# Kernel optimization log

Measured on AMD Instinct MI355X. Metric: run time of the kernel, lower is better.

## Reference

```python
import jax, jax.numpy as jnp
import numpy as np

N = 6144      # total residues (12 complexes x 512)
SEG = 512
NC = 14       # atom channels per residue
E = 64        # embed_size
HD = 128      # hidden_size
C = 25        # num_classes
K = 9         # k_neighbors
L = 3         # n_layers
ROUNDS = 3    # iter_round


def _forward(X, S, batch_id, embed, W_in, b_in, channel_w, eW1, eb1, eW2, eb2, cW1, cb1, cW2, cb2, nW1, nb1, nW2, nb2, mW1, mb1, mW2, mb2, oW1, ob1, oW2, ob2):
    n = X.shape[0]
    silu = jax.nn.silu
    # pairs in different complexes (or self) are never neighbors
    cross = (batch_id[:, None] != batch_id[None, :]) | jnp.eye(n, dtype=bool)
    Hmem = None
    H = None
    for t in range(ROUNDS):
        H0 = embed[S]                                    # residue embedding [N,E]
        if Hmem is not None:                             # keep_memory: memory_ffn(H_prev)
            m = silu(Hmem) @ mW1 + mb1
            H0 = H0 + (silu(m) @ mW2 + mb2)
        H = H0 @ W_in + b_in                             # [N,HD]
        # dynamic KNN edge construction on current CA coordinates (_knn_edges)
        ca = X[:, 1]                                     # [N,3]
        d2 = jnp.sum((ca[:, None, :] - ca[None, :, :]) ** 2, -1)
        d2 = jnp.where(cross, 1e9, d2)
        _, nbr = jax.lax.top_k(-d2, K)                   # [N,K] neighbor indices
        for l in range(L):                               # AMEGNN / AMEncoder layers
            Hj = H[nbr]                                  # gather [N,K,HD]
            Xj = X[nbr]                                  # gather [N,K,NC,3]
            diff = X[:, None] - Xj                       # [N,K,NC,3]
            # channel-weighted radial feature
            radial = jnp.einsum('nkcd,nkcd,c->nk', diff, diff, channel_w)[..., None]
            Hi = jnp.broadcast_to(H[:, None], Hj.shape)
            ein = jnp.concatenate([Hi, Hj, radial], -1)  # [N,K,2HD+1]
            msg = silu(silu(ein @ eW1[l] + eb1[l]) @ eW2[l] + eb2[l])
            scale = silu(msg @ cW1[l] + cb1[l]) @ cW2[l] + cb2[l]     # [N,K,1]
            X = X + jnp.mean(diff * scale[..., None], axis=1)        # equivariant coord update
            agg = jnp.sum(msg, axis=1)                   # scatter-sum over neighbors [N,HD]
            H = H + silu(jnp.concatenate([H, agg], -1) @ nW1[l] + nb1[l]) @ nW2[l] + nb2[l]
        Hmem = H
    logits = silu(silu(H) @ oW1 + ob1) @ oW2 + ob2       # ffn_residue
    return logits, X


def setup_inputs() -> dict:
    key = jax.random.key(0)
    ks = jax.random.split(key, 16)
    r = lambda i, shape, s=0.05: jax.random.normal(ks[i], shape, dtype=jnp.float32) * s
    return {
        'X': jax.random.normal(ks[0], (N, NC, 3), dtype=jnp.float32) * 3.0,
        'S': jax.random.randint(ks[1], (N,), 0, C),
        'batch_id': jnp.arange(N, dtype=jnp.int32) // SEG,
        'embed': r(2, (C, E), 1.0),
        'W_in': r(3, (E, HD)), 'b_in': jnp.zeros((HD,), jnp.float32),
        'channel_w': jax.random.uniform(ks[4], (NC,), dtype=jnp.float32),
        'eW1': r(5, (L, 2 * HD + 1, HD)), 'eb1': jnp.zeros((L, HD), jnp.float32),
        'eW2': r(6, (L, HD, HD)), 'eb2': jnp.zeros((L, HD), jnp.float32),
        'cW1': r(7, (L, HD, HD)), 'cb1': jnp.zeros((L, HD), jnp.float32),
        'cW2': r(8, (L, HD, 1)), 'cb2': jnp.zeros((L, 1), jnp.float32),
        'nW1': r(9, (L, 2 * HD, HD)), 'nb1': jnp.zeros((L, HD), jnp.float32),
        'nW2': r(10, (L, HD, HD)), 'nb2': jnp.zeros((L, HD), jnp.float32),
        'mW1': r(11, (HD, HD)), 'mb1': jnp.zeros((HD,), jnp.float32),
        'mW2': r(12, (HD, E)), 'mb2': jnp.zeros((E,), jnp.float32),
        'oW1': r(13, (HD, HD)), 'ob1': jnp.zeros((HD,), jnp.float32),
        'oW2': r(14, (HD, C)), 'ob2': jnp.zeros((C,), jnp.float32),
    }


def reference(X, S, batch_id, embed, W_in, b_in, channel_w, eW1, eb1, eW2, eb2, cW1, cb1, cW2, cb2, nW1, nb1, nW2, nb2, mW1, mb1, mW2, mb2, oW1, ob1, oW2, ob2):
    return _forward(X, S, batch_id, embed, W_in, b_in, channel_w, eW1, eb1, eW2, eb2, cW1, cb1, cW2, cb2, nW1, nb1, nW2, nb2, mW1, mb1, mW2, mb2, oW1, ob1, oW2, ob2)
```

## Files before the change

kernel.cpp:

```cpp
#include <hip/hip_runtime.h>
#include <math.h>

#define NNODE 6144
#define SEG   512
#define NCH   14
#define XD    42
#define ED    64
#define HD    128
#define NCLS  25
#define KN    9
#define NPB   7
#define ROWS  64
#define EDGE_BLOCKS ((NNODE + NPB - 1) / NPB)

typedef __attribute__((ext_vector_type(8))) short short8;
typedef __attribute__((ext_vector_type(4))) short short4v;
typedef __attribute__((ext_vector_type(4))) float f32x4;

__device__ __forceinline__ float silu_f(float x) {
  return x / (1.0f + __expf(-x));
}
__device__ __forceinline__ short f2bf(float x) {
  unsigned u = __builtin_bit_cast(unsigned, x);
  unsigned r = (u + 0x7fffu + ((u >> 16) & 1u)) >> 16;
  return (short)r;
}
__device__ __forceinline__ float bf2f(short s) {
  unsigned u = ((unsigned)(unsigned short)s) << 16;
  return __builtin_bit_cast(float, u);
}
__device__ __forceinline__ f32x4 mfma16(short8 a, short8 b, f32x4 c) {
  return __builtin_amdgcn_mfma_f32_16x16x32_bf16(a, b, c, 0, 0, 0);
}
__device__ __forceinline__ int swz128(int row, int col) {
  return row * 128 + (col ^ ((row & 7) << 3));
}
__device__ __forceinline__ int swz256(int row, int col) {
  return row * 256 + (col ^ ((row & 7) << 3));
}

__global__ __launch_bounds__(256) void prep_weights(
    const float* __restrict__ eW1, const float* __restrict__ eW2,
    const float* __restrict__ cW1, const float* __restrict__ nW1,
    const float* __restrict__ nW2, short* __restrict__ out)
{
  const int mat = blockIdx.y % 5, l = blockIdx.y / 5;
  const int idx = blockIdx.x * 256 + threadIdx.x;
  const int K = (mat == 0 || mat == 3) ? 256 : 128;
  if (idx >= K * 128) return;
  const int n = idx / K, k = idx - n * K;
  const float* src;
  switch (mat) {
    case 0: src = eW1 + (size_t)l * 257 * 128; break;
    case 1: src = eW2 + (size_t)l * 128 * 128; break;
    case 2: src = cW1 + (size_t)l * 128 * 128; break;
    case 3: src = nW1 + (size_t)l * 256 * 128; break;
    default: src = nW2 + (size_t)l * 128 * 128; break;
  }
  const int dofs[5] = {0, 32768, 49152, 65536, 98304};
  out[(size_t)l * 114688 + dofs[mat] + idx] = f2bf(src[k * 128 + n]);
}

__global__ void copy_kernel(const float* __restrict__ src, float* __restrict__ dst, int n) {
  int i = blockIdx.x * blockDim.x + threadIdx.x;
  if (i < n) dst[i] = src[i];
}

__global__ __launch_bounds__(512) void pq_kernel(
    const float* __restrict__ Hin, const short* __restrict__ W1T,
    float* __restrict__ PQ)
{
  __shared__ __align__(16) short A[32 * HD];
  const int t = threadIdx.x;
  const int m0 = blockIdx.x * 32;

  const float4* H4 = (const float4*)(Hin + (size_t)m0 * HD);
  for (int idx = t; idx < 32 * 32; idx += 512) {
    const int r = idx >> 5, c4 = idx & 31;
    float4 v = H4[r * 32 + c4];
    short4v s;
    s.x = f2bf(v.x); s.y = f2bf(v.y); s.z = f2bf(v.z); s.w = f2bf(v.w);
    *(short4v*)&A[swz128(r, c4 * 4)] = s;
  }
  __syncthreads();

  const int wid = t >> 6, lane = t & 63;
  const int lr = lane & 15, lk = lane >> 4;
  const int mt = wid >> 2;
  const int nb = (wid & 3) * 4;
  const int rA = mt * 16 + lr;

  f32x4 acc[4] = {};
#pragma unroll
  for (int ks = 0; ks < 4; ++ks) {
    const int k0 = ks * 32 + lk * 8;
    const short8 a = *(const short8*)&A[swz128(rA, k0)];
#pragma unroll
    for (int ni = 0; ni < 4; ++ni) {
      const int c = (nb + ni) * 16 + lr;
      const short* bp = (c < HD) ? (W1T + c * 256 + k0)
                                 : (W1T + (c - HD) * 256 + HD + k0);
      const short8 b = *(const short8*)bp;
      acc[ni] = mfma16(a, b, acc[ni]);
    }
  }
#pragma unroll
  for (int ni = 0; ni < 4; ++ni) {
    const int c = (nb + ni) * 16 + lr;
#pragma unroll
    for (int g = 0; g < 4; ++g) {
      const int row = mt * 16 + lk * 4 + g;
      PQ[(size_t)(m0 + row) * 256 + c] = acc[ni][g];
    }
  }
}

__global__ __launch_bounds__(128) void h_init_kernel(
    const float* __restrict__ embed, const int* __restrict__ S,
    const float* __restrict__ W_in, const float* __restrict__ b_in,
    const float* __restrict__ Hmem,
    const float* __restrict__ mW1, const float* __restrict__ mb1,
    const float* __restrict__ mW2, const float* __restrict__ mb2,
    float* __restrict__ Hout)
{
  __shared__ float a1[HD];
  __shared__ float a2[HD];
  __shared__ float h0[ED];
  const int i = blockIdx.x, j = threadIdx.x;

  if (Hmem) {
    a1[j] = silu_f(Hmem[i * HD + j]);
    __syncthreads();
    float m0 = 0.f, m1 = 0.f, m2 = 0.f, m3 = 0.f;
    for (int k = 0; k < HD; k += 4) {
      m0 = fmaf(a1[k + 0], mW1[(k + 0) * HD + j], m0);
      m1 = fmaf(a1[k + 1], mW1[(k + 1) * HD + j], m1);
      m2 = fmaf(a1[k + 2], mW1[(k + 2) * HD + j], m2);
      m3 = fmaf(a1[k + 3], mW1[(k + 3) * HD + j], m3);
    }
    a2[j] = silu_f(mb1[j] + ((m0 + m1) + (m2 + m3)));
    __syncthreads();
    if (j < ED) {
      float v0 = 0.f, v1 = 0.f, v2 = 0.f, v3 = 0.f;
      for (int k = 0; k < HD; k += 4) {
        v0 = fmaf(a2[k + 0], mW2[(k + 0) * ED + j], v0);
        v1 = fmaf(a2[k + 1], mW2[(k + 1) * ED + j], v1);
        v2 = fmaf(a2[k + 2], mW2[(k + 2) * ED + j], v2);
        v3 = fmaf(a2[k + 3], mW2[(k + 3) * ED + j], v3);
      }
      h0[j] = embed[S[i] * ED + j] + mb2[j] + ((v0 + v1) + (v2 + v3));
    }
  } else {
    if (j < ED) h0[j] = embed[S[i] * ED + j];
  }
  __syncthreads();
  float h0a = 0.f, h1a = 0.f, h2a = 0.f, h3a = 0.f;
  for (int k = 0; k < ED; k += 4) {
    h0a = fmaf(h0[k + 0], W_in[(k + 0) * HD + j], h0a);
    h1a = fmaf(h0[k + 1], W_in[(k + 1) * HD + j], h1a);
    h2a = fmaf(h0[k + 2], W_in[(k + 2) * HD + j], h2a);
    h3a = fmaf(h0[k + 3], W_in[(k + 3) * HD + j], h3a);
  }
  Hout[i * HD + j] = b_in[j] + ((h0a + h1a) + (h2a + h3a));
}

__global__ __launch_bounds__(256) void knn_kernel(const float* __restrict__ X,
                                                  int* __restrict__ nbr)
{
  const int w = threadIdx.x >> 6, lane = threadIdx.x & 63;
  const int i = blockIdx.x * 4 + w;
  const int base = (i / SEG) * SEG;

  const float cx = X[i * XD + 3], cy = X[i * XD + 4], cz = X[i * XD + 5];
  float dv[8];
  int   di[8];
#pragma unroll
  for (int q = 0; q < 8; ++q) {
    const int j = base + lane + q * 64;
    float dx = __fsub_rn(cx, X[j * XD + 3]);
    float dy = __fsub_rn(cy, X[j * XD + 4]);
    float dz = __fsub_rn(cz, X[j * XD + 5]);
    float d2 = __fadd_rn(__fadd_rn(__fmul_rn(dx, dx), __fmul_rn(dy, dy)), __fmul_rn(dz, dz));
    if (j == i) d2 = 1e9f;
    dv[q] = d2; di[q] = j;
  }
  for (int it = 0; it < KN; ++it) {
    float bv = dv[0]; int bi = di[0];
#pragma unroll
    for (int q = 1; q < 8; ++q)
      if (dv[q] < bv || (dv[q] == bv && di[q] < bi)) { bv = dv[q]; bi = di[q]; }
#pragma unroll
    for (int m = 1; m < 64; m <<= 1) {
      float ov = __shfl_xor(bv, m, 64);
      int   oi = __shfl_xor(bi, m, 64);
      if (ov < bv || (ov == bv && oi < bi)) { bv = ov; bi = oi; }
    }
    if (lane == 0) nbr[i * KN + it] = bi;
    const int rel = bi - base;
    const int oq = rel >> 6;
#pragma unroll
    for (int q = 0; q < 8; ++q)
      if (q == oq && (rel & 63) == lane) dv[q] = 3e38f;
  }
}

__global__ __launch_bounds__(512, 8) void edge_layer_kernel(
    const float* __restrict__ Hin,  float* __restrict__ Hout,
    const float* __restrict__ Xin,  float* __restrict__ Xout,
    const int*   __restrict__ nbr,  const float* __restrict__ channel_w,
    const float* __restrict__ PQ,
    const float* __restrict__ eW1,  const float* __restrict__ eb1,
    const float* __restrict__ eb2,  const float* __restrict__ cb1,
    const float* __restrict__ cW2,  const float* __restrict__ cb2,
    const float* __restrict__ nb1,  const float* __restrict__ nb2,
    const short* __restrict__ W2T,  const short* __restrict__ C1T,
    const short* __restrict__ N1T,  const short* __restrict__ N2T)
{
  __shared__ __align__(16) short bufA[ROWS * HD];
  __shared__ __align__(16) short bufB[ROWS * HD];
  __shared__ __align__(16) short nodeA[NPB * 256];
  __shared__ __align__(16) short uT[NPB * HD];
  __shared__ float XiS[NPB][XD];
  __shared__ float scaleS[ROWS];
  __shared__ int   nbrS[ROWS];

  const int t  = threadIdx.x;
  const int n0 = blockIdx.x * NPB;
  const int nvalid = (NNODE - n0 < NPB) ? (NNODE - n0) : NPB;
  const int evalid = nvalid * KN;

  {
    const int row  = t >> 3;
    const int part = t & 7;
    const bool rvalid = row < evalid;
    const int nd = row / KN;
    const int jn = rvalid ? nbr[n0 * KN + row] : n0;
    if (part == 0) nbrS[row] = jn;

    float r = 0.f;
    if (rvalid) {
      const float* xi = Xin + (size_t)(n0 + nd) * XD;
      const float* xj = Xin + (size_t)jn * XD;
      {
        const int c = part;
        float dx = xi[c * 3 + 0] - xj[c * 3 + 0];
        float dy = xi[c * 3 + 1] - xj[c * 3 + 1];
        float dz = xi[c * 3 + 2] - xj[c * 3 + 2];
        r += channel_w[c] * (dx * dx + dy * dy + dz * dz);
      }
      if (part < 6) {
        const int c = part + 8;
        float dx = xi[c * 3 + 0] - xj[c * 3 + 0];
        float dy = xi[c * 3 + 1] - xj[c * 3 + 1];
        float dz = xi[c * 3 + 2] - xj[c * 3 + 2];
        r += channel_w[c] * (dx * dx + dy * dy + dz * dz);
      }
    }
    r += __shfl_xor(r, 1, 64);
    r += __shfl_xor(r, 2, 64);
    r += __shfl_xor(r, 4, 64);

    {
      float* XiSf = &XiS[0][0];
      for (int idx = t; idx < NPB * XD; idx += 512) {
        const int nd2 = idx / XD;
        XiSf[idx] = (nd2 < nvalid) ? Xin[n0 * XD + idx] : 0.f;
      }
      for (int idx = t; idx < NPB * HD; idx += 512) {
        const int r2 = idx >> 7, c = idx & 127;
        const float v = (r2 < nvalid) ? Hin[(size_t)(n0 + r2) * HD + c] : 0.f;
        nodeA[swz256(r2, c)] = f2bf(v);
      }
    }

    const int inode = n0 + ((nd < nvalid) ? nd : 0);
    const float4* PQ4 = (const float4*)PQ;
    const float4* w2564 = (const float4*)(eW1 + 256 * HD);
    const float4* eb14 = (const float4*)eb1;
#pragma unroll
    for (int ii = 0; ii < 4; ++ii) {
      const int c4 = part + ii * 8;
      const float4 p = PQ4[(size_t)inode * 64 + c4];
      const float4 q = PQ4[(size_t)jn * 64 + 32 + c4];
      const float4 w = w2564[c4];
      const float4 bb = eb14[c4];
      short4v s;
      s.x = f2bf(silu_f(p.x + q.x + r * w.x + bb.x));
      s.y = f2bf(silu_f(p.y + q.y + r * w.y + bb.y));
      s.z = f2bf(silu_f(p.z + q.z + r * w.z + bb.z));
      s.w = f2bf(silu_f(p.w + q.w + r * w.w + bb.w));
      *(short4v*)&bufA[swz128(row, c4 * 4)] = s;
    }
  }
  __syncthreads();

  const int wid  = t >> 6;
  const int lane = t & 63;
  const int m2 = wid >> 2;
  const int n2 = wid & 3;
  const int lr = lane & 15;
  const int lk = lane >> 4;
  const int rA0 = (m2 * 2) * 16 + lr;
  const int rA1 = rA0 + 16;

  {
    f32x4 acc[2][2] = {};
    const short* b0p = W2T + ((n2 * 2) * 16 + lr) * 128;
    const short* b1p = b0p + 16 * 128;
#pragma unroll
    for (int ks = 0; ks < 4; ++ks) {
      const int k0 = ks * 32 + lk * 8;
      const short8 a0 = *(const short8*)&bufA[swz128(rA0, k0)];
      const short8 a1 = *(const short8*)&bufA[swz128(rA1, k0)];
      const short8 b0 = *(const short8*)(b0p + k0);
      const short8 b1 = *(const short8*)(b1p + k0);
      acc[0][0] = mfma16(a0, b0, acc[0][0]);
      acc[0][1] = mfma16(a0, b1, acc[0][1]);
      acc[1][0] = mfma16(a1, b0, acc[1][0]);
      acc[1][1] = mfma16(a1, b1, acc[1][1]);
    }
#pragma unroll
    for (int ni = 0; ni < 2; ++ni) {
      const int col = (n2 * 2 + ni) * 16 + lr;
      const float bias = eb2[col];
#pragma unroll
      for (int mi = 0; mi < 2; ++mi) {
        const int rb = (m2 * 2 + mi) * 16 + lk * 4;
#pragma unroll
        for (int g = 0; g < 4; ++g)
          bufB[swz128(rb + g, col)] = f2bf(silu_f(acc[mi][ni][g] + bias));
      }
    }
  }
  __syncthreads();

  {
    f32x4 acc[2][2] = {};
    const short* b0p = C1T + ((n2 * 2) * 16 + lr) * 128;
    const short* b1p = b0p + 16 * 128;
#pragma unroll
    for (int ks = 0; ks < 4; ++ks) {
      const int k0 = ks * 32 + lk * 8;
      const short8 a0 = *(const short8*)&bufB[swz128(rA0, k0)];
      const short8 a1 = *(const short8*)&bufB[swz128(rA1, k0)];
      const short8 b0 = *(const short8*)(b0p + k0);
      const short8 b1 = *(const short8*)(b1p + k0);
      acc[0][0] = mfma16(a0, b0, acc[0][0]);
      acc[0][1] = mfma16(a0, b1, acc[0][1]);
      acc[1][0] = mfma16(a1, b0, acc[1][0]);
      acc[1][1] = mfma16(a1, b1, acc[1][1]);
    }
#pragma unroll
    for (int ni = 0; ni < 2; ++ni) {
      const int col = (n2 * 2 + ni) * 16 + lr;
      const float bias = cb1[col];
#pragma unroll
      for (int mi = 0; mi < 2; ++mi) {
        const int rb = (m2 * 2 + mi) * 16 + lk * 4;
#pragma unroll
        for (int g = 0; g < 4; ++g)
          bufA[swz128(rb + g, col)] = f2bf(silu_f(acc[mi][ni][g] + bias));
      }
    }
  }
  __syncthreads();

  {
    const int row = t >> 3, part = t & 7;
    float s = 0.f;
#pragma unroll
    for (int qq = 0; qq < 16; ++qq) {
      const int k = part * 16 + qq;
      s = fmaf(bf2f(bufA[swz128(row, k)]), cW2[k], s);
    }
    s += __shfl_xor(s, 1, 64);
    s += __shfl_xor(s, 2, 64);
    s += __shfl_xor(s, 4, 64);
    if (part == 0) scaleS[row] = s + cb2[0];
  }
  for (int idx = t; idx < NPB * HD; idx += 512) {
    const int r2 = idx >> 7, col = idx & 127;
    float v = 0.f;
    if (r2 < nvalid) {
#pragma unroll
      for (int k = 0; k < KN; ++k) v += bf2f(bufB[swz128(r2 * KN + k, col)]);
    }
    nodeA[swz256(r2, col + HD)] = f2bf(v);
  }
  __syncthreads();

  {
    f32x4 acc = {};
    const short* bp = N1T + (wid * 16 + lr) * 256;
#pragma unroll
    for (int ks = 0; ks < 8; ++ks) {
      const int k0 = ks * 32 + lk * 8;
      short8 a = {0, 0, 0, 0, 0, 0, 0, 0};
      if (lr < NPB) a = *(const short8*)&nodeA[swz256(lr, k0)];
      const short8 b = *(const short8*)(bp + k0);
      acc = mfma16(a, b, acc);
    }
    const int col = wid * 16 + lr;
    const float bias = nb1[col];
#pragma unroll
    for (int g = 0; g < 4; ++g) {
      const int orow = lk * 4 + g;
      if (orow < NPB) uT[swz128(orow, col)] = f2bf(silu_f(acc[g] + bias));
    }
  }
  {
    float* XiSf = &XiS[0][0];
    for (int idx = t; idx < NPB * XD; idx += 512) {
      const int nd = idx / XD, e = idx - nd * XD;
      if (nd < nvalid) {
        const float xi = XiSf[idx];
        float a = 0.f;
#pragma unroll
        for (int k = 0; k < KN; ++k) {
          const int r = nd * KN + k;
          a += (xi - Xin[(size_t)nbrS[r] * XD + e]) * scaleS[r];
        }
        Xout[(size_t)(n0 + nd) * XD + e] = xi + a / 9.0f;
      }
    }
  }
  __syncthreads();

  {
    f32x4 acc = {};
    const short* bp = N2T + (wid * 16 + lr) * 128;
#pragma unroll
    for (int ks = 0; ks < 4; ++ks) {
      const int k0 = ks * 32 + lk * 8;
      short8 a = {0, 0, 0, 0, 0, 0, 0, 0};
      if (lr < NPB) a = *(const short8*)&uT[swz128(lr, k0)];
      const short8 b = *(const short8*)(bp + k0);
      acc = mfma16(a, b, acc);
    }
    const int col = wid * 16 + lr;
    const float bias = nb2[col];
#pragma unroll
    for (int g = 0; g < 4; ++g) {
      const int row = lk * 4 + g;
      if (row < nvalid)
        Hout[(size_t)(n0 + row) * HD + col] =
            Hin[(size_t)(n0 + row) * HD + col] + acc[g] + bias;
    }
  }
}

__global__ __launch_bounds__(128) void out_kernel(
    const float* __restrict__ H, const float* __restrict__ X,
    const float* __restrict__ oW1, const float* __restrict__ ob1,
    const float* __restrict__ oW2, const float* __restrict__ ob2,
    float* __restrict__ out)
{
  __shared__ float hs[HD];
  __shared__ float u[HD];
  const int i = blockIdx.x, j = threadIdx.x;

  hs[j] = silu_f(H[i * HD + j]);
  __syncthreads();
  float a0 = 0.f, a1 = 0.f, a2 = 0.f, a3 = 0.f;
  for (int k = 0; k < HD; k += 4) {
    a0 = fmaf(hs[k + 0], oW1[(k + 0) * HD + j], a0);
    a1 = fmaf(hs[k + 1], oW1[(k + 1) * HD + j], a1);
    a2 = fmaf(hs[k + 2], oW1[(k + 2) * HD + j], a2);
    a3 = fmaf(hs[k + 3], oW1[(k + 3) * HD + j], a3);
  }
  u[j] = silu_f(ob1[j] + ((a0 + a1) + (a2 + a3)));
  __syncthreads();
  if (j < NCLS) {
    float o0 = 0.f, o1 = 0.f, o2 = 0.f, o3 = 0.f;
    for (int k = 0; k < HD; k += 4) {
      o0 = fmaf(u[k + 0], oW2[(k + 0) * NCLS + j], o0);
      o1 = fmaf(u[k + 1], oW2[(k + 1) * NCLS + j], o1);
      o2 = fmaf(u[k + 2], oW2[(k + 2) * NCLS + j], o2);
      o3 = fmaf(u[k + 3], oW2[(k + 3) * NCLS + j], o3);
    }
    out[i * NCLS + j] = ob2[j] + ((o0 + o1) + (o2 + o3));
  }
  if (j < XD) out[NNODE * NCLS + i * XD + j] = X[i * XD + j];
}

extern "C" void kernel_launch(void* const* d_in, const int* in_sizes, int n_in,
                              void* d_out, int out_size, void* d_ws, size_t ws_size,
                              hipStream_t stream)
{
  const float* X0       = (const float*)d_in[0];
  const int*   S        = (const int*)  d_in[1];
  const float* embed    = (const float*)d_in[3];
  const float* W_in     = (const float*)d_in[4];
  const float* b_in     = (const float*)d_in[5];
  const float* channelw = (const float*)d_in[6];
  const float* eW1      = (const float*)d_in[7];
  const float* eb1      = (const float*)d_in[8];
  const float* eW2      = (const float*)d_in[9];
  const float* eb2      = (const float*)d_in[10];
  const float* cW1      = (const float*)d_in[11];
  const float* cb1      = (const float*)d_in[12];
  const float* cW2      = (const float*)d_in[13];
  const float* cb2      = (const float*)d_in[14];
  const float* nW1      = (const float*)d_in[15];
  const float* nb1      = (const float*)d_in[16];
  const float* nW2      = (const float*)d_in[17];
  const float* nb2      = (const float*)d_in[18];
  const float* mW1      = (const float*)d_in[19];
  const float* mb1      = (const float*)d_in[20];
  const float* mW2      = (const float*)d_in[21];
  const float* mb2      = (const float*)d_in[22];
  const float* oW1      = (const float*)d_in[23];
  const float* ob1      = (const float*)d_in[24];
  const float* oW2      = (const float*)d_in[25];
  const float* ob2      = (const float*)d_in[26];

  char* ws = (char*)d_ws;
  const size_t HBYTES = (size_t)NNODE * HD * sizeof(float);
  const size_t XBYTES = (size_t)NNODE * XD * sizeof(float);
  float* Hb[2] = { (float*)(ws), (float*)(ws + HBYTES) };
  float* Xb[2] = { (float*)(ws + 2 * HBYTES), (float*)(ws + 2 * HBYTES + XBYTES) };
  int*   nbr   = (int*)(ws + 2 * HBYTES + 2 * XBYTES);
  short* Wbf   = (short*)(ws + 2 * HBYTES + 2 * XBYTES + (size_t)NNODE * KN * sizeof(int));
  float* PQ    = (float*)(ws + 2 * HBYTES + 2 * XBYTES + (size_t)NNODE * KN * sizeof(int)
                             + 3 * 114688 * sizeof(short));

  prep_weights<<<dim3(128, 15), 256, 0, stream>>>(eW1, eW2, cW1, nW1, nW2, Wbf);
  copy_kernel<<<(NNODE * XD + 255) / 256, 256, 0, stream>>>(X0, Xb[0], NNODE * XD);

  int hc = 0, xc = 0;
  for (int t = 0; t < 3; ++t) {
    const float* Hmem = (t == 0) ? nullptr : Hb[hc];
    h_init_kernel<<<NNODE, HD, 0, stream>>>(embed, S, W_in, b_in, Hmem,
                                            mW1, mb1, mW2, mb2, Hb[hc ^ 1]);
    hc ^= 1;
    knn_kernel<<<NNODE / 4, 256, 0, stream>>>(Xb[xc], nbr);
    for (int l = 0; l < 3; ++l) {
      const short* Wl = Wbf + (size_t)l * 114688;
      pq_kernel<<<NNODE / 32, 512, 0, stream>>>(Hb[hc], Wl, PQ);
      edge_layer_kernel<<<EDGE_BLOCKS, 512, 0, stream>>>(
          Hb[hc], Hb[hc ^ 1], Xb[xc], Xb[xc ^ 1], nbr, channelw, PQ,
          eW1 + (size_t)l * 257 * HD, eb1 + (size_t)l * HD,
          eb2 + (size_t)l * HD,  cb1 + (size_t)l * HD,
          cW2 + (size_t)l * HD,  cb2 + (size_t)l,
          nb1 + (size_t)l * HD,  nb2 + (size_t)l * HD,
          Wl + 32768, Wl + 49152, Wl + 65536, Wl + 98304);
      hc ^= 1; xc ^= 1;
    }
  }
  out_kernel<<<NNODE, HD, 0, stream>>>(Hb[hc], Xb[xc], oW1, ob1, oW2, ob2, (float*)d_out);
}
```

Baseline: 610.1 us.

## Fuse coord-scale dot into C1 epilogue, shrink PQ tiles, vectorize node loads

The cW2 dot product that computes the per-edge coordinate scale is now folded into the cW1 MFMA epilogue. Each wave reduces its column slice with cross-lane shuffles and writes partial sums to a small shared array, so the bf16 hidden activations are no longer stored to LDS and the barrier before re-reading them is gone. The pq kernel uses 16-row tiles so twice as many blocks launch, and the edge kernel loads the node H rows as float4, drops the Xi shared staging (reading Xin directly), and relaxes launch bounds from (512,8) to 512. In exchange, more partial sums are summed at use time, the scale is computed in fp32 rather than from bf16-rounded activations, and the per-block bf16 weight traffic in pq doubles.

```diff
diff --git a/kernel.cpp b/kernel.cpp
--- a/kernel.cpp
+++ b/kernel.cpp
@@ -70,14 +70,13 @@
     const float* __restrict__ Hin, const short* __restrict__ W1T,
     float* __restrict__ PQ)
 {
-  __shared__ __align__(16) short A[32 * HD];
+  __shared__ __align__(16) short A[16 * HD];
   const int t = threadIdx.x;
-  const int m0 = blockIdx.x * 32;
-
-  const float4* H4 = (const float4*)(Hin + (size_t)m0 * HD);
-  for (int idx = t; idx < 32 * 32; idx += 512) {
-    const int r = idx >> 5, c4 = idx & 31;
-    float4 v = H4[r * 32 + c4];
+  const int m0 = blockIdx.x * 16;
+
+  {
+    const int r = t >> 5, c4 = t & 31;
+    const float4 v = ((const float4*)(Hin + (size_t)m0 * HD))[r * 32 + c4];
     short4v s;
     s.x = f2bf(v.x); s.y = f2bf(v.y); s.z = f2bf(v.z); s.w = f2bf(v.w);
     *(short4v*)&A[swz128(r, c4 * 4)] = s;
@@ -86,18 +85,15 @@
 
   const int wid = t >> 6, lane = t & 63;
   const int lr = lane & 15, lk = lane >> 4;
-  const int mt = wid >> 2;
-  const int nb = (wid & 3) * 4;
-  const int rA = mt * 16 + lr;
-
-  f32x4 acc[4] = {};
+
+  f32x4 acc[2] = {};
 #pragma unroll
   for (int ks = 0; ks < 4; ++ks) {
     const int k0 = ks * 32 + lk * 8;
-    const short8 a = *(const short8*)&A[swz128(rA, k0)];
-#pragma unroll
-    for (int ni = 0; ni < 4; ++ni) {
-      const int c = (nb + ni) * 16 + lr;
+    const short8 a = *(const short8*)&A[swz128(lr, k0)];
+#pragma unroll
+    for (int ni = 0; ni < 2; ++ni) {
+      const int c = (wid * 2 + ni) * 16 + lr;
       const short* bp = (c < HD) ? (W1T + c * 256 + k0)
                                  : (W1T + (c - HD) * 256 + HD + k0);
       const short8 b = *(const short8*)bp;
@@ -105,11 +101,11 @@
     }
   }
 #pragma unroll
-  for (int ni = 0; ni < 4; ++ni) {
-    const int c = (nb + ni) * 16 + lr;
+  for (int ni = 0; ni < 2; ++ni) {
+    const int c = (wid * 2 + ni) * 16 + lr;
 #pragma unroll
     for (int g = 0; g < 4; ++g) {
-      const int row = mt * 16 + lk * 4 + g;
+      const int row = lk * 4 + g;
       PQ[(size_t)(m0 + row) * 256 + c] = acc[ni][g];
     }
   }
@@ -204,7 +200,7 @@
   }
 }
 
-__global__ __launch_bounds__(512, 8) void edge_layer_kernel(
+__global__ __launch_bounds__(512) void edge_layer_kernel(
     const float* __restrict__ Hin,  float* __restrict__ Hout,
     const float* __restrict__ Xin,  float* __restrict__ Xout,
     const int*   __restrict__ nbr,  const float* __restrict__ channel_w,
@@ -220,8 +216,7 @@
   __shared__ __align__(16) short bufB[ROWS * HD];
   __shared__ __align__(16) short nodeA[NPB * 256];
   __shared__ __align__(16) short uT[NPB * HD];
-  __shared__ float XiS[NPB][XD];
-  __shared__ float scaleS[ROWS];
+  __shared__ float scalePart[ROWS][4];
   __shared__ int   nbrS[ROWS];
 
   const int t  = threadIdx.x;
@@ -260,17 +255,13 @@
     r += __shfl_xor(r, 2, 64);
     r += __shfl_xor(r, 4, 64);
 
-    {
-      float* XiSf = &XiS[0][0];
-      for (int idx = t; idx < NPB * XD; idx += 512) {
-        const int nd2 = idx / XD;
-        XiSf[idx] = (nd2 < nvalid) ? Xin[n0 * XD + idx] : 0.f;
-      }
-      for (int idx = t; idx < NPB * HD; idx += 512) {
-        const int r2 = idx >> 7, c = idx & 127;
-        const float v = (r2 < nvalid) ? Hin[(size_t)(n0 + r2) * HD + c] : 0.f;
-        nodeA[swz256(r2, c)] = f2bf(v);
-      }
+    if (t < NPB * (HD / 4)) {
+      const int r2 = t >> 5, c4 = t & 31;
+      float4 v = make_float4(0.f, 0.f, 0.f, 0.f);
+      if (r2 < nvalid) v = ((const float4*)Hin)[(size_t)(n0 + r2) * 32 + c4];
+      short4v s;
+      s.x = f2bf(v.x); s.y = f2bf(v.y); s.z = f2bf(v.z); s.w = f2bf(v.w);
+      *(short4v*)&nodeA[swz256(r2, c4 * 4)] = s;
     }
 
     const int inode = n0 + ((nd < nvalid) ? nd : 0);
@@ -350,33 +341,37 @@
       acc[1][0] = mfma16(a1, b0, acc[1][0]);
       acc[1][1] = mfma16(a1, b1, acc[1][1]);
     }
+    float p[2][4];
+#pragma unroll
+    for (int mi = 0; mi < 2; ++mi)
+#pragma unroll
+      for (int g = 0; g < 4; ++g) p[mi][g] = 0.f;
 #pragma unroll
     for (int ni = 0; ni < 2; ++ni) {
       const int col = (n2 * 2 + ni) * 16 + lr;
       const float bias = cb1[col];
-#pragma unroll
-      for (int mi = 0; mi < 2; ++mi) {
-        const int rb = (m2 * 2 + mi) * 16 + lk * 4;
+      const float wv = cW2[col];
+#pragma unroll
+      for (int mi = 0; mi < 2; ++mi)
 #pragma unroll
         for (int g = 0; g < 4; ++g)
-          bufA[swz128(rb + g, col)] = f2bf(silu_f(acc[mi][ni][g] + bias));
-      }
-    }
-  }
-  __syncthreads();
-
-  {
-    const int row = t >> 3, part = t & 7;
-    float s = 0.f;
-#pragma unroll
-    for (int qq = 0; qq < 16; ++qq) {
-      const int k = part * 16 + qq;
-      s = fmaf(bf2f(bufA[swz128(row, k)]), cW2[k], s);
-    }
-    s += __shfl_xor(s, 1, 64);
-    s += __shfl_xor(s, 2, 64);
-    s += __shfl_xor(s, 4, 64);
-    if (part == 0) scaleS[row] = s + cb2[0];
+          p[mi][g] = fmaf(silu_f(acc[mi][ni][g] + bias), wv, p[mi][g]);
+    }
+#pragma unroll
+    for (int m = 1; m < 16; m <<= 1) {
+#pragma unroll
+      for (int mi = 0; mi < 2; ++mi)
+#pragma unroll
+        for (int g = 0; g < 4; ++g)
+          p[mi][g] += __shfl_xor(p[mi][g], m, 64);
+    }
+    if (lr == 0) {
+#pragma unroll
+      for (int mi = 0; mi < 2; ++mi)
+#pragma unroll
+        for (int g = 0; g < 4; ++g)
+          scalePart[(m2 * 2 + mi) * 16 + lk * 4 + g][n2] = p[mi][g];
+    }
   }
   for (int idx = t; idx < NPB * HD; idx += 512) {
     const int r2 = idx >> 7, col = idx & 127;
@@ -409,16 +404,18 @@
     }
   }
   {
-    float* XiSf = &XiS[0][0];
+    const float c2 = cb2[0];
     for (int idx = t; idx < NPB * XD; idx += 512) {
       const int nd = idx / XD, e = idx - nd * XD;
       if (nd < nvalid) {
-        const float xi = XiSf[idx];
+        const float xi = Xin[(size_t)n0 * XD + idx];
         float a = 0.f;
 #pragma unroll
         for (int k = 0; k < KN; ++k) {
           const int r = nd * KN + k;
-          a += (xi - Xin[(size_t)nbrS[r] * XD + e]) * scaleS[r];
+          const float sc = ((scalePart[r][0] + scalePart[r][1])
+                          + (scalePart[r][2] + scalePart[r][3])) + c2;
+          a += (xi - Xin[(size_t)nbrS[r] * XD + e]) * sc;
         }
         Xout[(size_t)(n0 + nd) * XD + e] = xi + a / 9.0f;
       }
@@ -536,7 +533,7 @@
     knn_kernel<<<NNODE / 4, 256, 0, stream>>>(Xb[xc], nbr);
     for (int l = 0; l < 3; ++l) {
       const short* Wl = Wbf + (size_t)l * 114688;
-      pq_kernel<<<NNODE / 32, 512, 0, stream>>>(Hb[hc], Wl, PQ);
+      pq_kernel<<<NNODE / 16, 512, 0, stream>>>(Hb[hc], Wl, PQ);
       edge_layer_kernel<<<EDGE_BLOCKS, 512, 0, stream>>>(
           Hb[hc], Hb[hc ^ 1], Xb[xc], Xb[xc ^ 1], nbr, channelw, PQ,
           eW1 + (size_t)l * 257 * HD, eb1 + (size_t)l * HD,
```

Result: faster. 595.5 us (-2.4%).
